# Kernel optimization log

Hardware: AMD Instinct MI355X
Metric: run time of the kernel (lower is better)

Reference implementation:

```python
import jax, jax.numpy as jnp
import numpy as np


def _sobel_kernels():
    sx = np.array([[[-1, 0, 1], [-2, 0, 2], [-1, 0, 1]],
                   [[-2, 0, 2], [-4, 0, 4], [-2, 0, 2]],
                   [[-1, 0, 1], [-2, 0, 2], [-1, 0, 1]]], dtype=np.float32)
    sy = np.array([[[-1, -2, -1], [0, 0, 0], [1, 2, 1]],
                   [[-2, -4, -2], [0, 0, 0], [2, 4, 2]],
                   [[-1, -2, -1], [0, 0, 0], [1, 2, 1]]], dtype=np.float32)
    sz = np.array([[[1, 2, 1], [2, 4, 2], [1, 2, 1]],
                   [[0, 0, 0], [0, 0, 0], [0, 0, 0]],
                   [[-1, -2, -1], [-2, -4, -2], [-1, -2, -1]]], dtype=np.float32)
    # Stack as a single 3-output-channel conv: [O=3, I=1, 3, 3, 3]
    return jnp.asarray(np.stack([sx, sy, sz])[:, None])


def _conv3d(x, k):
    # x: [B, 1, D, H, W], k: [3, 1, 3, 3, 3] -> [B, 3, D, H, W]
    return jax.lax.conv_general_dilated(
        x, k, window_strides=(1, 1, 1), padding=[(1, 1)] * 3,
        dimension_numbers=('NCDHW', 'OIDHW', 'NCDHW'))


def setup_inputs() -> dict:
    key = jax.random.key(0)
    k1, k2 = jax.random.split(key)
    shape = (2, 1, 160, 192, 160)
    moved = jax.random.normal(k1, shape, dtype=jnp.float32)
    label = jax.random.normal(k2, shape, dtype=jnp.float32)
    return {"moved": moved, "label": label}


def reference(moved, label):
    k = _sobel_kernels()
    gm = _conv3d(moved, k)   # [B, 3, D, H, W]: x/y/z gradients
    gl = _conv3d(label, k)
    # per-direction L1 means (mean over B,D,H,W for each of the 3 channels)
    per_dir = jnp.mean(jnp.abs(gm - gl), axis=(0, 2, 3, 4))
    # original takes abs of each (already nonneg) loss, then averages
    return jnp.mean(jnp.abs(per_dir))
```

## Files before the change

kernel.cpp:

```cpp
#include <hip/hip_runtime.h>


#define BB 2
#define DD 160
#define HH 192
#define WW 160
#define HW (HH * WW)

#define TH 4
#define DC 8
#define NIT (DC + 2)
#define NTHREADS 256

__global__ __launch_bounds__(NTHREADS) void sobel_loss_kernel(
    const float* __restrict__ moved, const float* __restrict__ label,
    float* __restrict__ out)
{
    __shared__ float red[NTHREADS / 64];

    const int tid   = threadIdx.x;
    const int lane  = tid & 63;
    const int wavei = tid >> 6;
    const int wch   = blockIdx.x % 3;
    const int hgrp  = blockIdx.x / 3;
    const int hbase = (hgrp * 4 + wavei) * TH;
    const int d0    = blockIdx.y * DC;
    const int base_b = blockIdx.z * (DD * HW);

    const int  w0 = wch * 62;
    const int  w  = w0 + lane - 1;
    const bool wv = (unsigned)w < (unsigned)WW;
    const int  gw = min(max(w, 0), WW - 1);
    const bool outv = (lane >= 1) && (lane <= 62) && (w < WW);

    int  rowOff[TH + 2];
    bool rv[TH + 2];
#pragma unroll
    for (int r = 0; r < TH + 2; ++r) {
        const int gh = hbase - 1 + r;
        rv[r] = (unsigned)gh < (unsigned)HH;
        rowOff[r] = min(max(gh, 0), HH - 1) * WW + gw;
    }

    float mc[TH + 2], lc[TH + 2], mn[TH + 2], ln[TH + 2];
    {
        const int pb = base_b + max(d0 - 1, 0) * HW;
#pragma unroll
        for (int r = 0; r < TH + 2; ++r) {
            mc[r] = moved[pb + rowOff[r]];
            lc[r] = label[pb + rowOff[r]];
        }
    }

    float px1[TH], px2[TH], py1[TH], py2[TH], pz1[TH], pz2[TH];
#pragma unroll
    for (int i = 0; i < TH; ++i) {
        px1[i] = px2[i] = 0.f;
        py1[i] = py2[i] = 0.f;
        pz1[i] = pz2[i] = 0.f;
    }
    float acc = 0.f;

#pragma unroll
    for (int it = 0; it < NIT; ++it) {
        if (it + 1 < NIT) {
            const int pb = base_b + min(d0 + it, DD - 1) * HW;
#pragma unroll
            for (int r = 0; r < TH + 2; ++r) {
                mn[r] = moved[pb + rowOff[r]];
                ln[r] = label[pb + rowOff[r]];
            }
        }

        const bool pv = (unsigned)(d0 - 1 + it) < (unsigned)DD;
        float sW[TH + 2], dW[TH + 2];
#pragma unroll
        for (int r = 0; r < TH + 2; ++r) {
            const float d  = (pv && rv[r] && wv) ? (mc[r] - lc[r]) : 0.f;
            const float dl = __shfl_up(d, 1, 64);
            const float dr = __shfl_down(d, 1, 64);
            sW[r] = (dl + dr) + 2.f * d;
            dW[r] = dr - dl;
        }
#pragma unroll
        for (int i = 0; i < TH; ++i) {
            const float px = (dW[i] + dW[i + 2]) + 2.f * dW[i + 1];
            const float pz = (sW[i] + sW[i + 2]) + 2.f * sW[i + 1];
            const float py = sW[i + 2] - sW[i];
            if (it >= 2 && outv) {
                const float gx = px2[i] + 2.f * px1[i] + px;
                const float gy = py2[i] + 2.f * py1[i] + py;
                const float gz = pz2[i] - pz;
                acc += fabsf(gx) + fabsf(gy) + fabsf(gz);
            }
            px2[i] = px1[i]; px1[i] = px;
            py2[i] = py1[i]; py1[i] = py;
            pz2[i] = pz1[i]; pz1[i] = pz;
        }

#pragma unroll
        for (int r = 0; r < TH + 2; ++r) { mc[r] = mn[r]; lc[r] = ln[r]; }
    }

#pragma unroll
    for (int off = 32; off > 0; off >>= 1)
        acc += __shfl_down(acc, off, 64);
    if (lane == 0) red[wavei] = acc;
    __syncthreads();
    if (tid == 0) {
        const float s = red[0] + red[1] + red[2] + red[3];
        atomicAdd(out, s * (1.0f / (3.0f * BB * DD * HH * WW)));
    }
}

extern "C" void kernel_launch(void* const* d_in, const int* in_sizes, int n_in,
                              void* d_out, int out_size, void* d_ws, size_t ws_size,
                              hipStream_t stream) {
    const float* moved = (const float*)d_in[0];
    const float* label = (const float*)d_in[1];
    float* out = (float*)d_out;
    (void)in_sizes; (void)n_in; (void)out_size; (void)d_ws; (void)ws_size;

    hipMemsetAsync(out, 0, sizeof(float), stream);
    dim3 grid(36, DD / DC, BB);
    sobel_loss_kernel<<<grid, NTHREADS, 0, stream>>>(moved, label, out);
}
```

Before: 117.3 us.

## Use single-wave blocks with two-deep depth prefetch and longer depth chunks

Blocks shrink from four waves to one 64-thread wave, so the shared-memory reduction and __syncthreads disappear and each wave does its own atomicAdd. The depth loop now prefetches two slices ahead instead of one to hide more load latency, and the depth chunk grows from 8 to 10 slices to cut halo reloads. In exchange, register pressure rises, the grid has more blocks, and there are four times as many atomics on the single output.

```diff
diff --git a/kernel.cpp b/kernel.cpp
--- a/kernel.cpp
+++ b/kernel.cpp
@@ -8,22 +8,18 @@
 #define HW (HH * WW)
 
 #define TH 4
-#define DC 8
+#define DC 10
 #define NIT (DC + 2)
-#define NTHREADS 256
+#define NTHREADS 64
 
 __global__ __launch_bounds__(NTHREADS) void sobel_loss_kernel(
     const float* __restrict__ moved, const float* __restrict__ label,
     float* __restrict__ out)
 {
-    __shared__ float red[NTHREADS / 64];
-
-    const int tid   = threadIdx.x;
-    const int lane  = tid & 63;
-    const int wavei = tid >> 6;
+    const int lane  = threadIdx.x;
     const int wch   = blockIdx.x % 3;
-    const int hgrp  = blockIdx.x / 3;
-    const int hbase = (hgrp * 4 + wavei) * TH;
+    const int htile = blockIdx.x / 3;
+    const int hbase = htile * TH;
     const int d0    = blockIdx.y * DC;
     const int base_b = blockIdx.z * (DD * HW);
 
@@ -42,13 +38,16 @@
         rowOff[r] = min(max(gh, 0), HH - 1) * WW + gw;
     }
 
-    float mc[TH + 2], lc[TH + 2], mn[TH + 2], ln[TH + 2];
+    float mc[TH + 2], lc[TH + 2], mn[TH + 2], ln[TH + 2], m2[TH + 2], l2[TH + 2];
     {
-        const int pb = base_b + max(d0 - 1, 0) * HW;
+        const int pb0 = base_b + max(d0 - 1, 0) * HW;
+        const int pb1 = base_b + d0 * HW;
 #pragma unroll
         for (int r = 0; r < TH + 2; ++r) {
-            mc[r] = moved[pb + rowOff[r]];
-            lc[r] = label[pb + rowOff[r]];
+            mc[r] = moved[pb0 + rowOff[r]];
+            lc[r] = label[pb0 + rowOff[r]];
+            mn[r] = moved[pb1 + rowOff[r]];
+            ln[r] = label[pb1 + rowOff[r]];
         }
     }
 
@@ -63,12 +62,12 @@
 
 #pragma unroll
     for (int it = 0; it < NIT; ++it) {
-        if (it + 1 < NIT) {
-            const int pb = base_b + min(d0 + it, DD - 1) * HW;
+        if (it + 2 < NIT) {
+            const int pb = base_b + min(d0 + it + 1, DD - 1) * HW;
 #pragma unroll
             for (int r = 0; r < TH + 2; ++r) {
-                mn[r] = moved[pb + rowOff[r]];
-                ln[r] = label[pb + rowOff[r]];
+                m2[r] = moved[pb + rowOff[r]];
+                l2[r] = label[pb + rowOff[r]];
             }
         }
 
@@ -99,18 +98,17 @@
         }
 
 #pragma unroll
-        for (int r = 0; r < TH + 2; ++r) { mc[r] = mn[r]; lc[r] = ln[r]; }
+        for (int r = 0; r < TH + 2; ++r) {
+            mc[r] = mn[r]; lc[r] = ln[r];
+            mn[r] = m2[r]; ln[r] = l2[r];
+        }
     }
 
 #pragma unroll
     for (int off = 32; off > 0; off >>= 1)
         acc += __shfl_down(acc, off, 64);
-    if (lane == 0) red[wavei] = acc;
-    __syncthreads();
-    if (tid == 0) {
-        const float s = red[0] + red[1] + red[2] + red[3];
-        atomicAdd(out, s * (1.0f / (3.0f * BB * DD * HH * WW)));
-    }
+    if (lane == 0)
+        atomicAdd(out, acc * (1.0f / (3.0f * BB * DD * HH * WW)));
 }
 
 extern "C" void kernel_launch(void* const* d_in, const int* in_sizes, int n_in,
@@ -122,6 +120,6 @@
     (void)in_sizes; (void)n_in; (void)out_size; (void)d_ws; (void)ws_size;
 
     hipMemsetAsync(out, 0, sizeof(float), stream);
-    dim3 grid(36, DD / DC, BB);
+    dim3 grid(144, DD / DC, BB);
     sobel_loss_kernel<<<grid, NTHREADS, 0, stream>>>(moved, label, out);
 }
```

Result: slower. 158.8 us (+35.4%).

## Triple-buffer depth-plane loads with inline asm and manual vmcnt waits

Applied to the files above, without the earlier changes.

Replaces the double-buffered plane loads with a three-slot ring buffer filled through inline-asm global_load_dword. Two planes are prefetched before the loop and each iteration issues loads two planes ahead. A partial s_waitcnt vmcnt(24) waits only for the current plane, so more memory latency overlaps with compute. It also adds a waves_per_eu hint. This costs more registers and relies on hand-counted vmcnt values, which break if the compiler inserts or reorders other memory operations. It also performs extra, unused loads on the final iterations.

```diff
diff --git a/kernel.cpp b/kernel.cpp
--- a/kernel.cpp
+++ b/kernel.cpp
@@ -10,13 +10,20 @@
 #define TH 4
 #define DC 8
 #define NIT (DC + 2)
+#define NR (TH + 2)
 #define NTHREADS 256
 
-__global__ __launch_bounds__(NTHREADS) void sobel_loss_kernel(
-    const float* __restrict__ moved, const float* __restrict__ label,
-    float* __restrict__ out)
+#define GLOAD(dst, vo, sb) \
+    asm volatile("global_load_dword %0, %1, %2" \
+                 : "=v"(dst) : "v"(vo), "s"(sb) : "memory")
+
+__global__ __launch_bounds__(NTHREADS)
+__attribute__((amdgpu_waves_per_eu(1, 4)))
+void sobel_loss_kernel(const float* __restrict__ moved,
+                       const float* __restrict__ label,
+                       float* __restrict__ out)
 {
-    __shared__ float red[NTHREADS / 64];
+    __shared__ float red[4];
 
     const int tid   = threadIdx.x;
     const int lane  = tid & 63;
@@ -33,22 +40,31 @@
     const int  gw = min(max(w, 0), WW - 1);
     const bool outv = (lane >= 1) && (lane <= 62) && (w < WW);
 
-    int  rowOff[TH + 2];
-    bool rv[TH + 2];
+    int  voff[NR];
+    bool rv[NR];
 #pragma unroll
-    for (int r = 0; r < TH + 2; ++r) {
+    for (int r = 0; r < NR; ++r) {
         const int gh = hbase - 1 + r;
         rv[r] = (unsigned)gh < (unsigned)HH;
-        rowOff[r] = min(max(gh, 0), HH - 1) * WW + gw;
+        voff[r] = (min(max(gh, 0), HH - 1) * WW + gw) * 4;
     }
 
-    float mc[TH + 2], lc[TH + 2], mn[TH + 2], ln[TH + 2];
+    float bm[3][NR], bl[3][NR];
+
     {
-        const int pb = base_b + max(d0 - 1, 0) * HW;
+        const float* pm = moved + base_b + max(d0 - 1, 0) * HW;
+        const float* pl = label + base_b + max(d0 - 1, 0) * HW;
 #pragma unroll
-        for (int r = 0; r < TH + 2; ++r) {
-            mc[r] = moved[pb + rowOff[r]];
-            lc[r] = label[pb + rowOff[r]];
+        for (int r = 0; r < NR; ++r) {
+            GLOAD(bm[0][r], voff[r], pm);
+            GLOAD(bl[0][r], voff[r], pl);
+        }
+        const float* qm = moved + base_b + d0 * HW;
+        const float* ql = label + base_b + d0 * HW;
+#pragma unroll
+        for (int r = 0; r < NR; ++r) {
+            GLOAD(bm[1][r], voff[r], qm);
+            GLOAD(bl[1][r], voff[r], ql);
         }
     }
 
@@ -63,20 +79,31 @@
 
 #pragma unroll
     for (int it = 0; it < NIT; ++it) {
-        if (it + 1 < NIT) {
-            const int pb = base_b + min(d0 + it, DD - 1) * HW;
+        const int s  = it % 3;
+        const int s2 = (it + 2) % 3;
+
+        {
+            const int p = min(d0 + it + 1, DD - 1);
+            const float* pm = moved + base_b + p * HW;
+            const float* pl = label + base_b + p * HW;
 #pragma unroll
-            for (int r = 0; r < TH + 2; ++r) {
-                mn[r] = moved[pb + rowOff[r]];
-                ln[r] = label[pb + rowOff[r]];
+            for (int r = 0; r < NR; ++r) {
+                GLOAD(bm[s2][r], voff[r], pm);
+                GLOAD(bl[s2][r], voff[r], pl);
             }
         }
 
+        asm volatile("s_waitcnt vmcnt(24)"
+            : "+v"(bm[s][0]), "+v"(bm[s][1]), "+v"(bm[s][2]),
+              "+v"(bm[s][3]), "+v"(bm[s][4]), "+v"(bm[s][5]),
+              "+v"(bl[s][0]), "+v"(bl[s][1]), "+v"(bl[s][2]),
+              "+v"(bl[s][3]), "+v"(bl[s][4]), "+v"(bl[s][5]));
+
         const bool pv = (unsigned)(d0 - 1 + it) < (unsigned)DD;
-        float sW[TH + 2], dW[TH + 2];
+        float sW[NR], dW[NR];
 #pragma unroll
-        for (int r = 0; r < TH + 2; ++r) {
-            const float d  = (pv && rv[r] && wv) ? (mc[r] - lc[r]) : 0.f;
+        for (int r = 0; r < NR; ++r) {
+            const float d  = (pv && rv[r] && wv) ? (bm[s][r] - bl[s][r]) : 0.f;
             const float dl = __shfl_up(d, 1, 64);
             const float dr = __shfl_down(d, 1, 64);
             sW[r] = (dl + dr) + 2.f * d;
@@ -97,10 +124,9 @@
             py2[i] = py1[i]; py1[i] = py;
             pz2[i] = pz1[i]; pz1[i] = pz;
         }
+    }
 
-#pragma unroll
-        for (int r = 0; r < TH + 2; ++r) { mc[r] = mn[r]; lc[r] = ln[r]; }
-    }
+    asm volatile("s_waitcnt vmcnt(0)" ::: "memory");
 
 #pragma unroll
     for (int off = 32; off > 0; off >>= 1)
```

Result: no change. 116.6 us (-0.6%).
